# Optimization experiments

Measured on AMD Instinct MI355X. Metric: run time of the kernel, lower is better.

The kernel has to match this reference:

```python
import jax, jax.numpy as jnp
import numpy as np

N = 50000        # nodes
F = 128          # input feature dim
U = 128          # units (output dim)
E_RAND = 1_600_000  # random edges; N self-loops appended -> E = 1_650_000
LABEL_IDXS = np.array([0, 5, 17, 42], dtype=np.int32)  # label_idxs init arg (indices into F)


def setup_inputs() -> dict:
    key = jax.random.key(0)
    k1, k2, k3, k4, k5 = jax.random.split(key, 5)
    x = jax.random.normal(k1, (1, N, F), dtype=jnp.float32)
    src = jax.random.randint(k2, (E_RAND,), 0, N, dtype=jnp.int32)
    dst = jax.random.randint(k3, (E_RAND,), 0, N, dtype=jnp.int32)
    # append self-loops so the diagonal of A (Adiag term) is nontrivial,
    # matching a normalized Laplacian which always has diagonal entries
    loops = jnp.arange(N, dtype=jnp.int32)
    edge_src = jnp.concatenate([src, loops])
    edge_dst = jnp.concatenate([dst, loops])
    edge_w = jax.random.uniform(k4, (E_RAND + N,), dtype=jnp.float32)
    kernel = jax.random.normal(k5, (F, U), dtype=jnp.float32) * (1.0 / np.sqrt(F))
    bias = jnp.zeros((U,), dtype=jnp.float32)
    return {"x": x, "edge_src": edge_src, "edge_dst": edge_dst,
            "edge_w": edge_w, "kernel": kernel, "bias": bias}


def reference(x, edge_src, edge_dst, edge_w, kernel, bias):
    # x: [1, N, F]; sparse A given as COO edges (edge_src=row i, edge_dst=col j, edge_w=A[i,j])
    n = x.shape[1]
    xs = x[0]  # [N, F]
    # A @ X  (sparse matmul via gather + segment_sum)
    agg = jax.ops.segment_sum(edge_w[:, None] * xs[edge_dst], edge_src, num_segments=n)  # [N, F]
    # diag(A): entries where row == col
    diag = jax.ops.segment_sum(jnp.where(edge_src == edge_dst, edge_w, jnp.float32(0.0)),
                               edge_src, num_segments=n)  # [N]
    # B = sum_{i in label_idxs} e_i e_i^T is a diagonal 0/1 selector on feature columns,
    # so (Adiag @ X) @ B == diag[:,None] * (X * mask)
    mask = jnp.zeros((xs.shape[1],), xs.dtype).at[jnp.asarray(LABEL_IDXS)].set(1.0)  # [F]
    h = agg - diag[:, None] * (xs * mask)  # [N, F]
    out = jax.nn.relu(h @ kernel + bias)   # [N, U]
    return out[None]  # [1, N, U]
```

## Files before the change

### kernel.cpp

```cpp
#include <hip/hip_runtime.h>

#define FDIM 128
#define UDIM 128
#define BROWS 32
#define CAP   1408
#define TILE  4096
#define EPT   16
#define NPAIR 4

typedef __attribute__((ext_vector_type(8))) short short8;
typedef __attribute__((ext_vector_type(4))) float floatx4;

__device__ inline unsigned int round_bf16_bits(float a) {
  unsigned int ua = __float_as_uint(a);
  ua += 0x7fffu + ((ua >> 16) & 1u);
  return ua & 0xffff0000u;
}
__device__ inline unsigned int pack_bf16(float a, float b) {
  unsigned int ua = __float_as_uint(a);
  unsigned int ub = __float_as_uint(b);
  ua += 0x7fffu + ((ua >> 16) & 1u);
  ub += 0x7fffu + ((ub >> 16) & 1u);
  return (ua >> 16) | (ub & 0xffff0000u);
}

__global__ __launch_bounds__(256) void prep(
    const float* __restrict__ K, uint4* __restrict__ kfrag,
    int* __restrict__ zbase, int zcount) {
  int gid = blockIdx.x * 256 + threadIdx.x;
  if (gid < 2048) {
    int lane = gid & 63, bb = gid >> 6;
    int n = (bb >> 2) * 16 + (lane & 15);
    int k0 = (bb & 3) * 32 + (lane >> 4) * 8;
    unsigned int pq[4];
    #pragma unroll
    for (int j = 0; j < 4; ++j) {
      float a = K[(size_t)(k0 + 2 * j) * UDIM + n];
      float b = K[(size_t)(k0 + 2 * j + 1) * UDIM + n];
      pq[j] = pack_bf16(a, b);
    }
    kfrag[gid] = make_uint4(pq[0], pq[1], pq[2], pq[3]);
  }
  if (gid < zcount) zbase[gid] = 0;
}

__device__ void bin_dev(int blk, const int* __restrict__ src,
                        const int* __restrict__ dst, const float* __restrict__ w,
                        int* __restrict__ cursor, uint2* __restrict__ meta,
                        float* __restrict__ diag, int E, int NB, char* smem) {
  int* scnt  = (int*)smem;
  int* sbase = scnt + NB;
  int* scur  = sbase + NB;
  int t = threadIdx.x;
  for (int b = t; b < NB; b += 256) { scnt[b] = 0; scur[b] = 0; }
  __syncthreads();

  uint2 pay[EPT];
  int e0 = blk * TILE;
  #pragma unroll
  for (int j = 0; j < EPT; ++j) {
    int e = e0 + j * 256 + t;
    if (e < E) {
      int s = src[e];
      int d = dst[e];
      float wv = w[e];
      if (s == d) atomicAdd(&diag[s], wv);
      pay[j].x = round_bf16_bits(wv) | (unsigned int)d;
      pay[j].y = (unsigned int)s;
      atomicAdd(&scnt[s >> 5], 1);
    } else {
      pay[j].y = 0xffffffffu;
    }
  }
  __syncthreads();

  for (int b = t; b < NB; b += 256) {
    int c = scnt[b];
    if (c) sbase[b] = b * CAP + atomicAdd(&cursor[b], c);
  }
  __syncthreads();

  #pragma unroll
  for (int j = 0; j < EPT; ++j) {
    if (pay[j].y != 0xffffffffu) {
      int b = (int)(pay[j].y >> 5);
      int r = atomicAdd(&scur[b], 1);
      int pos = sbase[b] + r;
      if (pos < (b + 1) * CAP)
        meta[pos] = make_uint2(pay[j].x, pay[j].y & 31u);
    }
  }
}

__device__ void gemm_dev(int g, const float* __restrict__ x,
                         const uint4* __restrict__ kfrag,
                         unsigned short* __restrict__ Ybf, int N, char* smem) {
  unsigned short (*sX)[136] = (unsigned short (*)[136])smem;
  int t = threadIdx.x;
  int r0 = g * 64;

  #pragma unroll
  for (int i = 0; i < 8; ++i) {
    int li = i * 256 + t;
    int row = li >> 5;
    int col4 = (li & 31) * 4;
    int gr = r0 + row; if (gr > N - 1) gr = N - 1;
    float4 v = *(const float4*)(x + (size_t)gr * FDIM + col4);
    *(uint2*)(&sX[row][col4]) = make_uint2(pack_bf16(v.x, v.y), pack_bf16(v.z, v.w));
  }
  __syncthreads();

  int wave = t >> 6, lane = t & 63;
  int m = lane & 15, q = lane >> 4;

  short8 bf[2][4];
  #pragma unroll
  for (int c = 0; c < 2; ++c)
    #pragma unroll
    for (int ks = 0; ks < 4; ++ks)
      bf[c][ks] = *(const short8*)&kfrag[(size_t)((2 * wave + c) * 4 + ks) * 64 + lane];

  floatx4 acc[4][2];
  #pragma unroll
  for (int rt = 0; rt < 4; ++rt)
    #pragma unroll
    for (int c = 0; c < 2; ++c)
      acc[rt][c] = (floatx4){0.f, 0.f, 0.f, 0.f};

  #pragma unroll
  for (int ks = 0; ks < 4; ++ks) {
    #pragma unroll
    for (int rt = 0; rt < 4; ++rt) {
      short8 af = *(const short8*)&sX[rt * 16 + m][ks * 32 + q * 8];
      acc[rt][0] = __builtin_amdgcn_mfma_f32_16x16x32_bf16(af, bf[0][ks], acc[rt][0], 0, 0, 0);
      acc[rt][1] = __builtin_amdgcn_mfma_f32_16x16x32_bf16(af, bf[1][ks], acc[rt][1], 0, 0, 0);
    }
  }

  unsigned short* yp = Ybf + (size_t)wave * N * 32;
  #pragma unroll
  for (int rt = 0; rt < 4; ++rt) {
    #pragma unroll
    for (int c = 0; c < 2; ++c) {
      int off = c * 16 + m;
      #pragma unroll
      for (int reg = 0; reg < 4; ++reg) {
        int r = r0 + rt * 16 + q * 4 + reg;
        if (r < N)
          yp[(size_t)r * 32 + off] =
              (unsigned short)(round_bf16_bits(acc[rt][c][reg]) >> 16);
      }
    }
  }
}

__global__ __launch_bounds__(256) void bin_gemm(
    const int* __restrict__ src, const int* __restrict__ dst,
    const float* __restrict__ w, int* __restrict__ cursor,
    uint2* __restrict__ meta, float* __restrict__ diag,
    const float* __restrict__ x, const uint4* __restrict__ kfrag,
    unsigned short* __restrict__ Ybf, int N, int E, int NB, int nbin) {
  __shared__ alignas(16) char smem[18816];
  if (blockIdx.x < (unsigned)nbin)
    bin_dev(blockIdx.x, src, dst, w, cursor, meta, diag, E, NB, smem);
  else
    gemm_dev(blockIdx.x - nbin, x, kfrag, Ybf, N, smem);
}

__global__ __launch_bounds__(256) void sortk(
    const uint2* __restrict__ meta, const int* __restrict__ cursor,
    unsigned int* __restrict__ sortedg, int* __restrict__ rstartg,
    const float* __restrict__ diag, const float* __restrict__ x,
    float4* __restrict__ dscaleg, int N) {
  __shared__ unsigned int sdstw[CAP];
  __shared__ unsigned int sorted[CAP];
  __shared__ unsigned char skey[CAP];
  __shared__ int kcnt[BROWS];
  __shared__ int rstart[BROWS + 1];
  int b = blockIdx.x;
  int t = threadIdx.x;
  int cntE = cursor[b]; if (cntE > CAP) cntE = CAP;
  const uint2* mb = meta + (size_t)b * CAP;

  if (t < BROWS) {
    kcnt[t] = 0;
    int g = b * BROWS + t;
    if (g < N) {
      float dg = diag[g];
      dscaleg[g] = make_float4(dg * x[(size_t)g * FDIM + 0],
                               dg * x[(size_t)g * FDIM + 5],
                               dg * x[(size_t)g * FDIM + 17],
                               dg * x[(size_t)g * FDIM + 42]);
    }
  }
  __syncthreads();

  for (int e = t; e < cntE; e += 256) {
    uint2 m = mb[e];
    sdstw[e] = m.x;
    skey[e] = (unsigned char)m.y;
    atomicAdd(&kcnt[m.y & 31u], 1);
  }
  __syncthreads();

  if (t < BROWS) {
    int v = kcnt[t];
    int incl = v;
    #pragma unroll
    for (int off = 1; off < BROWS; off <<= 1) {
      int u = __shfl_up(incl, off, 64);
      if (t >= off) incl += u;
    }
    rstart[t + 1] = incl;
    kcnt[t] = incl - v;
    if (t == 0) rstart[0] = 0;
  }
  __syncthreads();

  for (int e = t; e < cntE; e += 256) {
    int k = skey[e];
    int pos = atomicAdd(&kcnt[k], 1);
    sorted[pos] = sdstw[e];
  }
  __syncthreads();

  unsigned int* sg = sortedg + (size_t)b * CAP;
  for (int e = t; e < cntE; e += 256) sg[e] = sorted[e];
  if (t < BROWS + 1) rstartg[b * (BROWS + 1) + t] = rstart[t];
}

__global__ __launch_bounds__(256, 8) void gather_slab(
    const unsigned short* __restrict__ Ybf, const unsigned int* __restrict__ sortedg,
    const int* __restrict__ rstartg, const float4* __restrict__ dscaleg,
    const float* __restrict__ K, const float* __restrict__ bias,
    float* __restrict__ out, int N) {
  __shared__ unsigned int srow[CAP];
  __shared__ int rsl[BROWS + 1];
  __shared__ float4 dsc[BROWS];
  int bi = blockIdx.x;
  int p = bi & 3;
  int b = bi >> 2;
  int t = threadIdx.x;
  int lane = t & 63, wave = t >> 6;
  int rs = lane >> 3;
  int fp = lane & 7;
  int r = wave * 8 + rs;
  int g = b * BROWS + r;

  if (t < BROWS + 1) rsl[t] = rstartg[b * (BROWS + 1) + t];
  if (t < BROWS) {
    int gg = b * BROWS + t;
    dsc[t] = (gg < N) ? dscaleg[gg] : make_float4(0.f, 0.f, 0.f, 0.f);
  }
  __syncthreads();
  int cnt = rsl[BROWS];

  const unsigned int* sg = sortedg + (size_t)b * CAP;
  for (int e = t; e < cnt; e += 256) srow[e] = sg[e];
  __syncthreads();

  const unsigned short* yp = Ybf + (size_t)p * N * 32;
  int base = rsl[r];
  int len = rsl[r + 1] - base;

  int ml = len;
  ml = max(ml, __shfl_xor(ml, 8, 64));
  ml = max(ml, __shfl_xor(ml, 16, 64));
  ml = max(ml, __shfl_xor(ml, 32, 64));

  float4 acc = {0.f, 0.f, 0.f, 0.f};
  for (int k = 0; k < ml; k += 2) {
    bool v0 = (k < len), v1 = (k + 1 < len);
    unsigned int w0 = srow[v0 ? base + k : 0];
    unsigned int w1 = srow[v1 ? base + k + 1 : 0];
    w0 = v0 ? w0 : 0u;
    w1 = v1 ? w1 : 0u;
    uint2 pk0 = *(const uint2*)(yp + (size_t)(w0 & 0xffffu) * 32 + fp * 4);
    uint2 pk1 = *(const uint2*)(yp + (size_t)(w1 & 0xffffu) * 32 + fp * 4);
    float wj0 = __uint_as_float(w0 & 0xffff0000u);
    float wj1 = __uint_as_float(w1 & 0xffff0000u);
    acc.x += wj0 * __uint_as_float(pk0.x << 16);
    acc.y += wj0 * __uint_as_float(pk0.x & 0xffff0000u);
    acc.z += wj0 * __uint_as_float(pk0.y << 16);
    acc.w += wj0 * __uint_as_float(pk0.y & 0xffff0000u);
    acc.x += wj1 * __uint_as_float(pk1.x << 16);
    acc.y += wj1 * __uint_as_float(pk1.x & 0xffff0000u);
    acc.z += wj1 * __uint_as_float(pk1.y << 16);
    acc.w += wj1 * __uint_as_float(pk1.y & 0xffff0000u);
  }

  if (g < N) {
    float4 ds = dsc[r];
    const int lf[4] = {0, 5, 17, 42};
    float dsv[4] = {ds.x, ds.y, ds.z, ds.w};
    #pragma unroll
    for (int tt = 0; tt < 4; ++tt) {
      float4 k4 = *(const float4*)(K + (size_t)lf[tt] * UDIM + p * 32 + fp * 4);
      acc.x -= dsv[tt] * k4.x; acc.y -= dsv[tt] * k4.y;
      acc.z -= dsv[tt] * k4.z; acc.w -= dsv[tt] * k4.w;
    }
    float4 b4 = *(const float4*)(bias + p * 32 + fp * 4);
    acc.x = fmaxf(acc.x + b4.x, 0.f);
    acc.y = fmaxf(acc.y + b4.y, 0.f);
    acc.z = fmaxf(acc.z + b4.z, 0.f);
    acc.w = fmaxf(acc.w + b4.w, 0.f);
    *(float4*)(out + (size_t)g * UDIM + p * 32 + fp * 4) = acc;
  }
}

extern "C" void kernel_launch(void* const* d_in, const int* in_sizes, int n_in,
                              void* d_out, int out_size, void* d_ws, size_t ws_size,
                              hipStream_t stream) {
  const float* x    = (const float*)d_in[0];
  const int*   esrc = (const int*)d_in[1];
  const int*   edst = (const int*)d_in[2];
  const float* ew   = (const float*)d_in[3];
  const float* K    = (const float*)d_in[4];
  const float* bias = (const float*)d_in[5];
  float* out = (float*)d_out;

  const int N = in_sizes[0] / FDIM;
  const int E = in_sizes[1];
  const int NB = (N + BROWS - 1) / BROWS;

  char* p = (char*)d_ws;
  unsigned short* Ybf = (unsigned short*)p; p += (size_t)N * UDIM * 2;
  float* diag  = (float*)p;         p += (size_t)N * 4;
  int*   cursor = (int*)p;          p += (size_t)NB * 4;
  uint4* kfrag = (uint4*)p;         p += (size_t)32 * 64 * 16;
  uint2* meta = (uint2*)p;          p += (size_t)NB * CAP * 8;
  unsigned int* sortedg = (unsigned int*)p; p += (size_t)NB * CAP * 4;
  int* rstartg = (int*)p;           p += (size_t)NB * (BROWS + 2) * 4;
  p = (char*)(((uintptr_t)p + 15) & ~(uintptr_t)15);
  float4* dscaleg = (float4*)p;     p += (size_t)N * 16;

  const int nbin = (E + TILE - 1) / TILE;
  const int ngemm = (N + 63) / 64;

  prep<<<(N + NB + 255) / 256, 256, 0, stream>>>(K, kfrag, (int*)diag, N + NB);
  bin_gemm<<<nbin + ngemm, 256, 0, stream>>>(
      esrc, edst, ew, cursor, meta, diag, x, kfrag, Ybf, N, E, NB, nbin);
  sortk<<<NB, 256, 0, stream>>>(meta, cursor, sortedg, rstartg,
                                diag, x, dscaleg, N);
  gather_slab<<<NB * NPAIR, 256, 0, stream>>>(
      Ybf, sortedg, rstartg, dscaleg, K, bias, out, N);
}
```

Measured before the change: 180.0 us.

## Sort rows by degree within each block to balance gather wave loop lengths

The sort kernel now runs a bitonic sort over the 32 rows of each block, keyed by edge count, and stores the resulting permutation. The gather kernel maps each 8-row wave group through this permutation, so rows of similar length share a wavefront and the per-wave max loop length comes closer to the average. The shared-memory staging copy is also widened to 16-byte loads, and the accumulators are split into 2-wide float vectors to allow packed FMA. The extra permutation buffer and sort add a little work to sortk.

```diff
diff --git a/kernel.cpp b/kernel.cpp
--- a/kernel.cpp
+++ b/kernel.cpp
@@ -10,6 +10,7 @@
 
 typedef __attribute__((ext_vector_type(8))) short short8;
 typedef __attribute__((ext_vector_type(4))) float floatx4;
+typedef __attribute__((ext_vector_type(2))) float f32x2;
 
 __device__ inline unsigned int round_bf16_bits(float a) {
   unsigned int ua = __float_as_uint(a);
@@ -170,6 +171,7 @@
 __global__ __launch_bounds__(256) void sortk(
     const uint2* __restrict__ meta, const int* __restrict__ cursor,
     unsigned int* __restrict__ sortedg, int* __restrict__ rstartg,
+    int* __restrict__ permg,
     const float* __restrict__ diag, const float* __restrict__ x,
     float4* __restrict__ dscaleg, int N) {
   __shared__ unsigned int sdstw[CAP];
@@ -203,17 +205,34 @@
   }
   __syncthreads();
 
-  if (t < BROWS) {
-    int v = kcnt[t];
-    int incl = v;
-    #pragma unroll
-    for (int off = 1; off < BROWS; off <<= 1) {
-      int u = __shfl_up(incl, off, 64);
-      if (t >= off) incl += u;
-    }
-    rstart[t + 1] = incl;
-    kcnt[t] = incl - v;
-    if (t == 0) rstart[0] = 0;
+  if (t < 64) {
+    int v = (t < BROWS) ? kcnt[t] : 0;
+    if (t < BROWS) {
+      int incl = v;
+      #pragma unroll
+      for (int off = 1; off < BROWS; off <<= 1) {
+        int u = __shfl_up(incl, off, 64);
+        if (t >= off) incl += u;
+      }
+      rstart[t + 1] = incl;
+      kcnt[t] = incl - v;
+      if (t == 0) rstart[0] = 0;
+    }
+    int lane = t;
+    int key = (t < BROWS) ? ((v << 6) | t) : -1;
+    #pragma unroll
+    for (int k = 2; k <= 32; k <<= 1) {
+      #pragma unroll
+      for (int j = k >> 1; j > 0; j >>= 1) {
+        int other = __shfl_xor(key, j, 64);
+        bool up = ((lane & k) == 0);
+        bool takeBig = ((lane & j) == 0);
+        bool keep = up ? (takeBig ? key >= other : key <= other)
+                       : (takeBig ? key <= other : key >= other);
+        key = keep ? key : other;
+      }
+    }
+    if (t < BROWS) permg[b * BROWS + t] = key & 63;
   }
   __syncthreads();
 
@@ -231,11 +250,13 @@
 
 __global__ __launch_bounds__(256, 8) void gather_slab(
     const unsigned short* __restrict__ Ybf, const unsigned int* __restrict__ sortedg,
-    const int* __restrict__ rstartg, const float4* __restrict__ dscaleg,
+    const int* __restrict__ rstartg, const int* __restrict__ permg,
+    const float4* __restrict__ dscaleg,
     const float* __restrict__ K, const float* __restrict__ bias,
     float* __restrict__ out, int N) {
-  __shared__ unsigned int srow[CAP];
+  __shared__ alignas(16) unsigned int srow[CAP];
   __shared__ int rsl[BROWS + 1];
+  __shared__ int sperm[BROWS];
   __shared__ float4 dsc[BROWS];
   int bi = blockIdx.x;
   int p = bi & 3;
@@ -244,11 +265,10 @@
   int lane = t & 63, wave = t >> 6;
   int rs = lane >> 3;
   int fp = lane & 7;
-  int r = wave * 8 + rs;
-  int g = b * BROWS + r;
 
   if (t < BROWS + 1) rsl[t] = rstartg[b * (BROWS + 1) + t];
   if (t < BROWS) {
+    sperm[t] = permg[b * BROWS + t];
     int gg = b * BROWS + t;
     dsc[t] = (gg < N) ? dscaleg[gg] : make_float4(0.f, 0.f, 0.f, 0.f);
   }
@@ -256,9 +276,14 @@
   int cnt = rsl[BROWS];
 
   const unsigned int* sg = sortedg + (size_t)b * CAP;
-  for (int e = t; e < cnt; e += 256) srow[e] = sg[e];
-  __syncthreads();
-
+  int nc4 = cnt >> 2;
+  for (int i = t; i < nc4; i += 256)
+    ((uint4*)srow)[i] = ((const uint4*)sg)[i];
+  for (int e = nc4 * 4 + t; e < cnt; e += 256) srow[e] = sg[e];
+  __syncthreads();
+
+  int r = sperm[wave * 8 + rs];
+  int g = b * BROWS + r;
   const unsigned short* yp = Ybf + (size_t)p * N * 32;
   int base = rsl[r];
   int len = rsl[r + 1] - base;
@@ -268,7 +293,7 @@
   ml = max(ml, __shfl_xor(ml, 16, 64));
   ml = max(ml, __shfl_xor(ml, 32, 64));
 
-  float4 acc = {0.f, 0.f, 0.f, 0.f};
+  f32x2 acc01 = {0.f, 0.f}, acc23 = {0.f, 0.f};
   for (int k = 0; k < ml; k += 2) {
     bool v0 = (k < len), v1 = (k + 1 < len);
     unsigned int w0 = srow[v0 ? base + k : 0];
@@ -279,17 +304,19 @@
     uint2 pk1 = *(const uint2*)(yp + (size_t)(w1 & 0xffffu) * 32 + fp * 4);
     float wj0 = __uint_as_float(w0 & 0xffff0000u);
     float wj1 = __uint_as_float(w1 & 0xffff0000u);
-    acc.x += wj0 * __uint_as_float(pk0.x << 16);
-    acc.y += wj0 * __uint_as_float(pk0.x & 0xffff0000u);
-    acc.z += wj0 * __uint_as_float(pk0.y << 16);
-    acc.w += wj0 * __uint_as_float(pk0.y & 0xffff0000u);
-    acc.x += wj1 * __uint_as_float(pk1.x << 16);
-    acc.y += wj1 * __uint_as_float(pk1.x & 0xffff0000u);
-    acc.z += wj1 * __uint_as_float(pk1.y << 16);
-    acc.w += wj1 * __uint_as_float(pk1.y & 0xffff0000u);
+    f32x2 wv0 = {wj0, wj0}, wv1 = {wj1, wj1};
+    f32x2 a0 = {__uint_as_float(pk0.x << 16), __uint_as_float(pk0.x & 0xffff0000u)};
+    f32x2 a1 = {__uint_as_float(pk0.y << 16), __uint_as_float(pk0.y & 0xffff0000u)};
+    f32x2 b0 = {__uint_as_float(pk1.x << 16), __uint_as_float(pk1.x & 0xffff0000u)};
+    f32x2 b1 = {__uint_as_float(pk1.y << 16), __uint_as_float(pk1.y & 0xffff0000u)};
+    acc01 += wv0 * a0;
+    acc23 += wv0 * a1;
+    acc01 += wv1 * b0;
+    acc23 += wv1 * b1;
   }
 
   if (g < N) {
+    float4 acc = make_float4(acc01[0], acc01[1], acc23[0], acc23[1]);
     float4 ds = dsc[r];
     const int lf[4] = {0, 5, 17, 42};
     float dsv[4] = {ds.x, ds.y, ds.z, ds.w};
@@ -331,6 +358,7 @@
   uint2* meta = (uint2*)p;          p += (size_t)NB * CAP * 8;
   unsigned int* sortedg = (unsigned int*)p; p += (size_t)NB * CAP * 4;
   int* rstartg = (int*)p;           p += (size_t)NB * (BROWS + 2) * 4;
+  int* permg = (int*)p;             p += (size_t)NB * BROWS * 4;
   p = (char*)(((uintptr_t)p + 15) & ~(uintptr_t)15);
   float4* dscaleg = (float4*)p;     p += (size_t)N * 16;
 
@@ -340,8 +368,8 @@
   prep<<<(N + NB + 255) / 256, 256, 0, stream>>>(K, kfrag, (int*)diag, N + NB);
   bin_gemm<<<nbin + ngemm, 256, 0, stream>>>(
       esrc, edst, ew, cursor, meta, diag, x, kfrag, Ybf, N, E, NB, nbin);
-  sortk<<<NB, 256, 0, stream>>>(meta, cursor, sortedg, rstartg,
+  sortk<<<NB, 256, 0, stream>>>(meta, cursor, sortedg, rstartg, permg,
                                 diag, x, dscaleg, N);
   gather_slab<<<NB * NPAIR, 256, 0, stream>>>(
-      Ybf, sortedg, rstartg, dscaleg, K, bias, out, N);
-}
+      Ybf, sortedg, rstartg, permg, dscaleg, K, bias, out, N);
+}
```

Result: faster. 175.7 us (-2.4%).
